# Performance work log

Hardware: AMD Instinct MI355X
Metric: run time of the kernel (lower is better)

The kernel has to match this reference:

```python
import jax, jax.numpy as jnp
import numpy as np
import math

D_MODEL = 1024
NUM_HEADS = 16
D_K = D_MODEL // NUM_HEADS
SEQ = 4096
THETA = 10000.0


def _rope_tables(d_k, max_seq_len, theta):
    freqs = 1.0 / theta ** (jnp.arange(0, d_k, 2, dtype=jnp.float32) / d_k)  # (d_k/2,)
    pos = jnp.arange(max_seq_len, dtype=jnp.float32)
    ang = pos[:, None] * freqs[None, :]  # (S, d_k/2)
    return jnp.cos(ang), jnp.sin(ang)


def setup_inputs() -> dict:
    key = jax.random.key(0)
    ks = jax.random.split(key, 5)
    std = math.sqrt(2.0 / (D_MODEL + D_MODEL))
    def trunc_w(k):
        return jax.random.truncated_normal(k, -3.0, 3.0, (D_MODEL, D_MODEL), jnp.float32) * std
    x = jax.random.normal(ks[0], (1, SEQ, D_MODEL), jnp.float32)
    Wq, Wk, Wv, Wo = trunc_w(ks[1]), trunc_w(ks[2]), trunc_w(ks[3]), trunc_w(ks[4])
    cos, sin = _rope_tables(D_K, SEQ, THETA)
    positions = jnp.arange(SEQ, dtype=jnp.int32)
    return {"x": x, "Wq": Wq, "Wk": Wk, "Wv": Wv, "Wo": Wo,
            "cos": cos, "sin": sin, "positions": positions}


def _apply_rope(t, cos, sin, positions):
    # t: (b, h, s, d_k); cos/sin: (max_s, d_k/2)
    c = cos[positions][None, None]  # (1,1,s,d_k/2)
    s = sin[positions][None, None]
    x1, x2 = t[..., ::2], t[..., 1::2]
    rotated = jnp.stack([x1 * c - x2 * s, x1 * s + x2 * c], axis=-1)  # (b,h,s,d_k/2,2)
    return rotated.reshape(t.shape)


def reference(x, Wq, Wk, Wv, Wo, cos, sin, positions):
    b, s, d = x.shape
    h, dk = NUM_HEADS, D_K
    def proj(W):
        y = jnp.einsum('bsi,oi->bso', x, W)
        return y.reshape(b, s, h, dk).transpose(0, 2, 1, 3)  # (b,h,s,dk)
    Q, K, V = proj(Wq), proj(Wk), proj(Wv)
    Q = _apply_rope(Q, cos, sin, positions)
    K = _apply_rope(K, cos, sin, positions)
    scores = jnp.einsum('bhqd,bhkd->bhqk', Q, K) / math.sqrt(dk)
    causal = jnp.tril(jnp.ones((s, s), dtype=bool))
    scores = jnp.where(causal[None, None], scores, -jnp.inf)
    weights = jax.nn.softmax(scores, axis=-1)
    y = jnp.einsum('bhqk,bhkd->bhqd', weights, V)
    y = y.transpose(0, 2, 1, 3).reshape(b, s, d)
    return jnp.einsum('bsi,oi->bso', y, Wo)
```

## Files before the change

kernel.cpp:

```cpp
#include <hip/hip_runtime.h>
#include <math.h>

#define SEQ 4096
#define DM  1024
#define NH  16
#define DK  64

typedef __attribute__((ext_vector_type(4))) float f32x4;
typedef __attribute__((ext_vector_type(8))) short bf16x8;
typedef __attribute__((ext_vector_type(8))) unsigned short u16x8;

union FragU { u16x8 u; bf16x8 b; ushort4 q[2]; unsigned w[4]; };

__device__ __forceinline__ unsigned cvtpk(float a, float b) {
    unsigned r; asm("v_cvt_pk_bf16_f32 %0, %1, %2" : "=v"(r) : "v"(a), "v"(b)); return r;
}
__device__ __forceinline__ float fexp2(float x) {
    float r; asm("v_exp_f32 %0, %1" : "=v"(r) : "v"(x)); return r;
}
__device__ __forceinline__ float bf_f(unsigned short s) {
    return __uint_as_float(((unsigned)s) << 16);
}
__device__ __forceinline__ void split4(float4 v, ushort4& hv, ushort4& lv) {
    union { ushort4 q; unsigned w[2]; } H, L;
    H.w[0] = cvtpk(v.x, v.y); H.w[1] = cvtpk(v.z, v.w);
    const float rx = v.x - __uint_as_float(H.w[0] << 16);
    const float ry = v.y - __uint_as_float(H.w[0] & 0xffff0000u);
    const float rz = v.z - __uint_as_float(H.w[1] << 16);
    const float rw = v.w - __uint_as_float(H.w[1] & 0xffff0000u);
    L.w[0] = cvtpk(rx, ry); L.w[1] = cvtpk(rz, rw);
    hv = H.q; lv = L.q;
}
__device__ __forceinline__ void split1(float f, unsigned short& h, unsigned short& l) {
    const unsigned hw = cvtpk(f, f) & 0xffffu;
    h = (unsigned short)hw;
    const float r = f - __uint_as_float(hw << 16);
    l = (unsigned short)(__float_as_uint(r) >> 16);
}

__global__ __launch_bounds__(256)
void split_f32(const float* __restrict__ src, unsigned short* __restrict__ hi,
               unsigned short* __restrict__ lo, int n4)
{
    const int stride = gridDim.x * 256;
    for (int i = blockIdx.x * 256 + threadIdx.x; i < n4; i += stride) {
        const float4 v = reinterpret_cast<const float4*>(src)[i];
        ushort4 hv, lv;
        split4(v, hv, lv);
        reinterpret_cast<ushort4*>(hi)[i] = hv;
        reinterpret_cast<ushort4*>(lo)[i] = lv;
    }
}

template<int MODE>
__global__ __launch_bounds__(256, 2)
void gemm_mfma(const unsigned short* __restrict__ Ahi, const unsigned short* __restrict__ Alo,
               const float* __restrict__ W0, const float* __restrict__ W1,
               const float* __restrict__ W2,
               unsigned short* __restrict__ OQh, unsigned short* __restrict__ OQl,
               unsigned short* __restrict__ OKh, unsigned short* __restrict__ OKl,
               unsigned short* __restrict__ OVh,
               float* __restrict__ Ofp,
               const float* __restrict__ cosT, const float* __restrict__ sinT,
               const int* __restrict__ positions)
{
    constexpr int NT = (MODE == 4) ? 24 : 8;
    __shared__ unsigned short As[128][76];
    __shared__ unsigned short Bs[128][76];

    const int t   = threadIdx.x;
    const int bid = blockIdx.x;
    const int qpx = (32 * NT) >> 3;
    const int swz = (bid & 7) * qpx + (bid >> 3);
    const int by  = swz / NT;
    const int bxf = swz % NT;
    const int wt  = (MODE == 4) ? (bxf >> 3) : 0;
    const int bx  = (MODE == 4) ? (bxf & 7) : bxf;
    const int m0  = by * 128;
    const float* W = (MODE == 4) ? (wt == 0 ? W0 : (wt == 1 ? W1 : W2)) : W0;

    const int lane = t & 63, w = t >> 6;
    const int wr = w >> 1, wc = w & 1;
    const int l15 = lane & 15, lg = lane >> 4;

    const int ar = t >> 1, ah = t & 1;
    const unsigned short* Aph = &Ahi[(size_t)(m0 + ar) * DM + ah * 16];
    const unsigned short* Apl = &Alo[(size_t)(m0 + ar) * DM + ah * 16];
    const float* Wp = &W[(size_t)(bx * 128 + ar) * DM + ah * 16];

    f32x4 acc[4][4];
#pragma unroll
    for (int mi = 0; mi < 4; ++mi)
#pragma unroll
        for (int ni = 0; ni < 4; ++ni) acc[mi][ni] = (f32x4){0.f, 0.f, 0.f, 0.f};

    float4 pb[4];
    u16x8 pah[2], pal[2];
    pah[0] = *reinterpret_cast<const u16x8*>(Aph);
    pah[1] = *reinterpret_cast<const u16x8*>(Aph + 8);
    pal[0] = *reinterpret_cast<const u16x8*>(Apl);
    pal[1] = *reinterpret_cast<const u16x8*>(Apl + 8);
#pragma unroll
    for (int g = 0; g < 4; ++g) pb[g] = *reinterpret_cast<const float4*>(Wp + g * 4);

    for (int kt = 0; kt < 32; ++kt) {
        {
            FragU h0, h1, l0, l1;
            h0.u = pah[0]; h1.u = pah[1]; l0.u = pal[0]; l1.u = pal[1];
            *reinterpret_cast<ushort4*>(&As[ar][0  + 4 * ah]) = h0.q[0];
            *reinterpret_cast<ushort4*>(&As[ar][8  + 4 * ah]) = h0.q[1];
            *reinterpret_cast<ushort4*>(&As[ar][16 + 4 * ah]) = h1.q[0];
            *reinterpret_cast<ushort4*>(&As[ar][24 + 4 * ah]) = h1.q[1];
            *reinterpret_cast<ushort4*>(&As[ar][32 + 4 * ah]) = l0.q[0];
            *reinterpret_cast<ushort4*>(&As[ar][40 + 4 * ah]) = l0.q[1];
            *reinterpret_cast<ushort4*>(&As[ar][48 + 4 * ah]) = l1.q[0];
            *reinterpret_cast<ushort4*>(&As[ar][56 + 4 * ah]) = l1.q[1];
        }
#pragma unroll
        for (int g = 0; g < 4; ++g) {
            ushort4 hv, lv;
            split4(pb[g], hv, lv);
            *reinterpret_cast<ushort4*>(&Bs[ar][8 * g + 4 * ah])      = hv;
            *reinterpret_cast<ushort4*>(&Bs[ar][32 + 8 * g + 4 * ah]) = lv;
        }
        __syncthreads();

        if (kt < 31) {
            const int ko = (kt + 1) * 32;
            pah[0] = *reinterpret_cast<const u16x8*>(Aph + ko);
            pah[1] = *reinterpret_cast<const u16x8*>(Aph + ko + 8);
            pal[0] = *reinterpret_cast<const u16x8*>(Apl + ko);
            pal[1] = *reinterpret_cast<const u16x8*>(Apl + ko + 8);
#pragma unroll
            for (int g = 0; g < 4; ++g)
                pb[g] = *reinterpret_cast<const float4*>(Wp + ko + g * 4);
        }

        FragU b_h[4], b_l[4];
#pragma unroll
        for (int ni = 0; ni < 4; ++ni) {
            const int row = wc * 64 + ni * 16 + l15;
            b_h[ni].u = *reinterpret_cast<const u16x8*>(&Bs[row][8 * lg]);
            b_l[ni].u = *reinterpret_cast<const u16x8*>(&Bs[row][32 + 8 * lg]);
        }
#pragma unroll
        for (int mi = 0; mi < 4; ++mi) {
            FragU a_h, a_l;
            const int row = wr * 64 + mi * 16 + l15;
            a_h.u = *reinterpret_cast<const u16x8*>(&As[row][8 * lg]);
            a_l.u = *reinterpret_cast<const u16x8*>(&As[row][32 + 8 * lg]);
#pragma unroll
            for (int ni = 0; ni < 4; ++ni) {
                f32x4 c = acc[mi][ni];
                c = __builtin_amdgcn_mfma_f32_16x16x32_bf16(a_h.b, b_h[ni].b, c, 0, 0, 0);
                c = __builtin_amdgcn_mfma_f32_16x16x32_bf16(a_h.b, b_l[ni].b, c, 0, 0, 0);
                c = __builtin_amdgcn_mfma_f32_16x16x32_bf16(a_l.b, b_h[ni].b, c, 0, 0, 0);
                acc[mi][ni] = c;
            }
        }
        __syncthreads();
    }

    if constexpr (MODE == 0) {
#pragma unroll
        for (int mi = 0; mi < 4; ++mi)
#pragma unroll
            for (int ni = 0; ni < 4; ++ni)
#pragma unroll
                for (int r = 0; r < 4; ++r) {
                    const int m = m0 + wr * 64 + mi * 16 + lg * 4 + r;
                    const int n = bx * 128 + wc * 64 + ni * 16 + l15;
                    Ofp[(size_t)m * DM + n] = acc[mi][ni][r];
                }
    } else if (wt == 2) {
#pragma unroll
        for (int mi = 0; mi < 4; ++mi)
#pragma unroll
            for (int ni = 0; ni < 4; ++ni) {
                ushort4 hv;
                unsigned short* hp_ = (unsigned short*)&hv;
#pragma unroll
                for (int r = 0; r < 4; ++r)
                    hp_[r] = (unsigned short)(cvtpk(acc[mi][ni][r], acc[mi][ni][r]) & 0xffffu);
                const int vrow = bx * 128 + wc * 64 + ni * 16 + l15;
                const size_t off = (size_t)vrow * SEQ + m0 + wr * 64 + mi * 16 + lg * 4;
                *reinterpret_cast<ushort4*>(&OVh[off]) = hv;
            }
    } else {
        unsigned short* Oh = (wt == 0) ? OQh : OKh;
        unsigned short* Ol = (wt == 0) ? OQl : OKl;
        const int head = bx * 2 + wc;
        const float qsc = 0.1803368801f;
#pragma unroll
        for (int mi = 0; mi < 4; ++mi)
#pragma unroll
            for (int r = 0; r < 4; ++r) {
                const int m   = m0 + wr * 64 + mi * 16 + lg * 4 + r;
                const int pos = positions[m];
#pragma unroll
                for (int ni = 0; ni < 4; ++ni) {
                    float val = acc[mi][ni][r];
                    const int d = ni * 16 + l15;
                    const float other = __shfl_xor(val, 1);
                    const float cc = cosT[pos * 32 + ni * 8 + (l15 >> 1)];
                    const float ss = sinT[pos * 32 + ni * 8 + (l15 >> 1)];
                    val = (d & 1) ? fmaf(other, ss, val * cc)
                                  : fmaf(other, -ss, val * cc);
                    if (wt == 0) val *= qsc;
                    unsigned short hh, ll;
                    split1(val, hh, ll);
                    const size_t off = ((size_t)head * SEQ + m) * DK + d;
                    Oh[off] = hh; Ol[off] = ll;
                }
            }
    }
}

__global__ __launch_bounds__(256, 2)
void attn_mfma(const unsigned short* __restrict__ Qhi, const unsigned short* __restrict__ Qlo,
               const unsigned short* __restrict__ Khi, const unsigned short* __restrict__ Klo,
               const unsigned short* __restrict__ Vhi,
               unsigned short* __restrict__ Yh, unsigned short* __restrict__ Yl,
               unsigned short* __restrict__ Pb,
               float2* __restrict__ mlA, float2* __restrict__ mlB)
{
    __shared__ unsigned short KsH[2][64][64], KsL[2][64][64], Vs[2][64][64];

    const int t = threadIdx.x, lane = t & 63, w = t >> 6;
    const int bid  = blockIdx.x;
    const int xcd  = bid & 7;
    const int s    = bid >> 3;
    const int hl   = s & 1;
    const int slot = s >> 1;
    const int p    = slot & 15;
    const int half = slot >> 4;
    const int h    = 2 * xcd + hl;

    const int l15 = lane & 15, lg = lane >> 4, dg = lg * 4;
    const int srow = t >> 2, q16 = t & 3;
    const int wh = w & 1;

    int wcol[4];
#pragma unroll
    for (int m = 0; m < 4; ++m) {
        const int g = (q16 >> 1) * 4 + m;
        wcol[m] = (((g ^ (srow & 7)) << 3) + ((q16 & 1) << 2));
    }

    u16x8 pf[6];
    auto PREFETCH = [&](int ktn) {
        const size_t gK = ((size_t)h * SEQ + (size_t)ktn * 64 + srow) * DK + q16 * 16;
        const size_t gV = ((size_t)h * DK + srow) * SEQ + (size_t)ktn * 64 + q16 * 16;
        pf[0] = *reinterpret_cast<const u16x8*>(&Khi[gK]);
        pf[1] = *reinterpret_cast<const u16x8*>(&Khi[gK + 8]);
        pf[2] = *reinterpret_cast<const u16x8*>(&Klo[gK]);
        pf[3] = *reinterpret_cast<const u16x8*>(&Klo[gK + 8]);
        pf[4] = *reinterpret_cast<const u16x8*>(&Vhi[gV]);
        pf[5] = *reinterpret_cast<const u16x8*>(&Vhi[gV + 8]);
    };
    auto STAGE = [&](int b) {
        FragU f;
        f.u = pf[0];
        *reinterpret_cast<ushort4*>(&KsH[b][srow][wcol[0]]) = f.q[0];
        *reinterpret_cast<ushort4*>(&KsH[b][srow][wcol[1]]) = f.q[1];
        f.u = pf[1];
        *reinterpret_cast<ushort4*>(&KsH[b][srow][wcol[2]]) = f.q[0];
        *reinterpret_cast<ushort4*>(&KsH[b][srow][wcol[3]]) = f.q[1];
        f.u = pf[2];
        *reinterpret_cast<ushort4*>(&KsL[b][srow][wcol[0]]) = f.q[0];
        *reinterpret_cast<ushort4*>(&KsL[b][srow][wcol[1]]) = f.q[1];
        f.u = pf[3];
        *reinterpret_cast<ushort4*>(&KsL[b][srow][wcol[2]]) = f.q[0];
        *reinterpret_cast<ushort4*>(&KsL[b][srow][wcol[3]]) = f.q[1];
        f.u = pf[4];
        *reinterpret_cast<ushort4*>(&Vs[b][srow][wcol[0]]) = f.q[0];
        *reinterpret_cast<ushort4*>(&Vs[b][srow][wcol[1]]) = f.q[1];
        f.u = pf[5];
        *reinterpret_cast<ushort4*>(&Vs[b][srow][wcol[2]]) = f.q[0];
        *reinterpret_cast<ushort4*>(&Vs[b][srow][wcol[3]]) = f.q[1];
    };

    const int nph = (half == 0) ? 2 : 1;
#pragma unroll 1
    for (int ph = 0; ph < nph; ++ph) {
        const int qt    = (half == 0 && ph == 0) ? p : (31 - p);
        const int kt0   = (half == 1) ? (31 - 2 * p) : 0;
        const int kt1   = (half == 0) ? ((ph == 0) ? (2 * p + 2) : (31 - 2 * p))
                                      : (64 - 2 * p);
        const int emode = (half == 0) ? ph : 2;
        const int diagkt = 2 * qt + (w >> 1);

        bf16x8 qh[2][2], ql[2][2];
#pragma unroll
        for (int u = 0; u < 2; ++u) {
            const size_t qrow = ((size_t)h * SEQ + (size_t)qt * 128 + w * 32 + u * 16 + l15) * DK;
#pragma unroll
            for (int c = 0; c < 2; ++c) {
                FragU uh, ul;
                uh.q[0] = *reinterpret_cast<const ushort4*>(&Qhi[qrow + c * 32 + dg]);
                uh.q[1] = *reinterpret_cast<const ushort4*>(&Qhi[qrow + c * 32 + 16 + dg]);
                ul.q[0] = *reinterpret_cast<const ushort4*>(&Qlo[qrow + c * 32 + dg]);
                ul.q[1] = *reinterpret_cast<const ushort4*>(&Qlo[qrow + c * 32 + 16 + dg]);
                qh[u][c] = uh.b; ql[u][c] = ul.b;
            }
        }

        f32x4 yacc[2][4];
#pragma unroll
        for (int u = 0; u < 2; ++u)
#pragma unroll
            for (int dt = 0; dt < 4; ++dt) yacc[u][dt] = (f32x4){0.f, 0.f, 0.f, 0.f};
        float m_run[2] = {-1e30f, -1e30f}, l_run[2] = {0.f, 0.f};

        PREFETCH(kt0);
        __syncthreads();
        STAGE(0);
        if (kt0 + 1 < kt1) PREFETCH(kt0 + 1);

        for (int kt = kt0; kt < kt1; ++kt) {
            const int b = (kt - kt0) & 1;
            __syncthreads();
            if (kt + 1 < kt1) {
                STAGE(b ^ 1);
                if (kt + 2 < kt1) PREFETCH(kt + 2);
            }

            if (kt <= diagkt) {
                const bool diag = (kt == diagkt);

                f32x4 st[2][4];
#pragma unroll
                for (int ktile = 0; ktile < 4; ++ktile) {
                    const int rowK = ktile * 16 + l15;
                    const int swk  = rowK & 7;
                    FragU kh0, kl0, kh1, kl1;
                    {
                        const int p0 = ((0 + lg) ^ swk) << 3;
                        const int p1 = ((4 + lg) ^ swk) << 3;
                        kh0.u = *reinterpret_cast<const u16x8*>(&KsH[b][rowK][p0]);
                        kl0.u = *reinterpret_cast<const u16x8*>(&KsL[b][rowK][p0]);
                        kh1.u = *reinterpret_cast<const u16x8*>(&KsH[b][rowK][p1]);
                        kl1.u = *reinterpret_cast<const u16x8*>(&KsL[b][rowK][p1]);
                    }
#pragma unroll
                    for (int u = 0; u < 2; ++u) {
                        if (diag && ktile > wh * 2 + u) {
                            st[u][ktile] = (f32x4){-1e30f, -1e30f, -1e30f, -1e30f};
                            continue;
                        }
                        f32x4 s0 = (f32x4){0.f, 0.f, 0.f, 0.f};
                        s0 = __builtin_amdgcn_mfma_f32_16x16x32_bf16(kh0.b, qh[u][0], s0, 0, 0, 0);
                        s0 = __builtin_amdgcn_mfma_f32_16x16x32_bf16(kh0.b, ql[u][0], s0, 0, 0, 0);
                        s0 = __builtin_amdgcn_mfma_f32_16x16x32_bf16(kl0.b, qh[u][0], s0, 0, 0, 0);
                        s0 = __builtin_amdgcn_mfma_f32_16x16x32_bf16(kh1.b, qh[u][1], s0, 0, 0, 0);
                        s0 = __builtin_amdgcn_mfma_f32_16x16x32_bf16(kh1.b, ql[u][1], s0, 0, 0, 0);
                        s0 = __builtin_amdgcn_mfma_f32_16x16x32_bf16(kl1.b, qh[u][1], s0, 0, 0, 0);
                        st[u][ktile] = s0;
                    }
                }

                if (diag) {
#pragma unroll
                    for (int u = 0; u < 2; ++u) {
                        const int ub = wh * 2 + u;
#pragma unroll
                        for (int r = 0; r < 4; ++r)
                            if (dg + r > l15) st[u][ub][r] = -1e30f;
                    }
                }

                bf16x8 pa[2][2];
#pragma unroll
                for (int u = 0; u < 2; ++u) {
                    float rowmax = st[u][0][0];
#pragma unroll
                    for (int ktile = 0; ktile < 4; ++ktile)
#pragma unroll
                        for (int r = 0; r < 4; ++r) rowmax = fmaxf(rowmax, st[u][ktile][r]);
                    rowmax = fmaxf(rowmax, __shfl_xor(rowmax, 16));
                    rowmax = fmaxf(rowmax, __shfl_xor(rowmax, 32));
                    if (!__all(rowmax <= m_run[u] + 11.5f)) {
                        const float mnew = fmaxf(m_run[u], rowmax);
                        const float factor = fexp2(m_run[u] - mnew);
                        l_run[u] *= factor;
#pragma unroll
                        for (int r = 0; r < 4; ++r) {
                            const float fr = __shfl(factor, (lg << 2) | r);
#pragma unroll
                            for (int dt = 0; dt < 4; ++dt) yacc[u][dt][r] *= fr;
                        }
                        m_run[u] = mnew;
                    }
                    float pp[4][4]; float psum = 0.f;
#pragma unroll
                    for (int ktile = 0; ktile < 4; ++ktile)
#pragma unroll
                        for (int r = 0; r < 4; ++r) {
                            pp[ktile][r] = fexp2(st[u][ktile][r] - m_run[u]);
                            psum += pp[ktile][r];
                        }
                    psum += __shfl_xor(psum, 16);
                    psum += __shfl_xor(psum, 32);
                    l_run[u] += psum;
#pragma unroll
                    for (int c = 0; c < 2; ++c) {
                        FragU P;
                        P.w[0] = cvtpk(pp[2 * c][0],     pp[2 * c][1]);
                        P.w[1] = cvtpk(pp[2 * c][2],     pp[2 * c][3]);
                        P.w[2] = cvtpk(pp[2 * c + 1][0], pp[2 * c + 1][1]);
                        P.w[3] = cvtpk(pp[2 * c + 1][2], pp[2 * c + 1][3]);
                        pa[u][c] = P.b;
                    }
                }

#pragma unroll
                for (int dt = 0; dt < 4; ++dt) {
                    const int rowV = dt * 16 + l15;
                    const int swv  = rowV & 7;
#pragma unroll
                    for (int c = 0; c < 2; ++c) {
                        FragU vh;
                        vh.u = *reinterpret_cast<const u16x8*>(&Vs[b][rowV][((c * 4 + lg) ^ swv) << 3]);
#pragma unroll
                        for (int u = 0; u < 2; ++u) {
                            if (diag && c == 1 && (wh * 2 + u) < 2) continue;
                            yacc[u][dt] = __builtin_amdgcn_mfma_f32_16x16x32_bf16(pa[u][c], vh.b, yacc[u][dt], 0, 0, 0);
                        }
                    }
                }
            }
        }

        if (emode == 0) {
#pragma unroll
            for (int u = 0; u < 2; ++u) {
                const float inv = 1.0f / l_run[u];
#pragma unroll
                for (int r = 0; r < 4; ++r) {
                    const float ir = __shfl(inv, (lg << 2) | r);
                    const size_t row = (size_t)qt * 128 + w * 32 + u * 16 + lg * 4 + r;
#pragma unroll
                    for (int dt = 0; dt < 4; ++dt) {
                        unsigned short hh, ll;
                        split1(yacc[u][dt][r] * ir, hh, ll);
                        const size_t off = row * DM + h * DK + dt * 16 + l15;
                        Yh[off] = hh; Yl[off] = ll;
                    }
                }
            }
        } else if (emode == 1) {
#pragma unroll
            for (int u = 0; u < 2; ++u) {
#pragma unroll
                for (int r = 0; r < 4; ++r) {
                    const size_t row = (size_t)qt * 128 + w * 32 + u * 16 + lg * 4 + r;
#pragma unroll
                    for (int dt = 0; dt < 4; ++dt) {
                        unsigned short hh, ll;
                        split1(yacc[u][dt][r], hh, ll);
                        const size_t off = row * DM + h * DK + dt * 16 + l15;
                        Yh[off] = hh; Yl[off] = ll;
                    }
                }
                if (lane < 16)
                    mlA[(h * 16 + p) * 128 + w * 32 + u * 16 + lane] =
                        make_float2(m_run[u], l_run[u]);
            }
        } else {
#pragma unroll
            for (int u = 0; u < 2; ++u) {
#pragma unroll
                for (int r = 0; r < 4; ++r) {
                    const int rloc = w * 32 + u * 16 + lg * 4 + r;
#pragma unroll
                    for (int dt = 0; dt < 4; ++dt) {
                        Pb[((size_t)(h * 16 + p) * 128 + rloc) * 64 + dt * 16 + l15] =
                            (unsigned short)(cvtpk(yacc[u][dt][r], yacc[u][dt][r]) & 0xffffu);
                    }
                }
                if (lane < 16)
                    mlB[(h * 16 + p) * 128 + w * 32 + u * 16 + lane] =
                        make_float2(m_run[u], l_run[u]);
            }
        }
    }
}

__global__ __launch_bounds__(256)
void merge_heavy(unsigned short* __restrict__ Yh, unsigned short* __restrict__ Yl,
                 const unsigned short* __restrict__ Pb,
                 const float2* __restrict__ mlA, const float2* __restrict__ mlB)
{
    const int hp = blockIdx.x;
    const int h = hp >> 4, p = hp & 15;
    const int t = threadIdx.x;
    const int row = t >> 1;
    const int d0 = (t & 1) * 32;
    const float2 a = mlA[hp * 128 + row];
    const float2 b = mlB[hp * 128 + row];
    const float m  = fmaxf(a.x, b.x);
    const float fA = fexp2(a.x - m), fB = fexp2(b.x - m);
    const float inv = 1.0f / (fA * a.y + fB * b.y);
    const size_t rg = ((size_t)(31 - p) * 128 + row) * DM + h * DK + d0;
    const size_t pg = ((size_t)hp * 128 + row) * 64 + d0;
#pragma unroll
    for (int dd = 0; dd < 32; dd += 8) {
        u16x8 vh = *reinterpret_cast<const u16x8*>(&Yh[rg + dd]);
        u16x8 vl = *reinterpret_cast<const u16x8*>(&Yl[rg + dd]);
        u16x8 vb = *reinterpret_cast<const u16x8*>(&Pb[pg + dd]);
        u16x8 oh, ol;
#pragma unroll
        for (int j = 0; j < 8; ++j) {
            const float ya = bf_f(vh[j]) + bf_f(vl[j]);
            const float yb = bf_f(vb[j]);
            const float o  = (fA * ya + fB * yb) * inv;
            unsigned short hh, ll;
            split1(o, hh, ll);
            oh[j] = hh; ol[j] = ll;
        }
        *reinterpret_cast<u16x8*>(&Yh[rg + dd]) = oh;
        *reinterpret_cast<u16x8*>(&Yl[rg + dd]) = ol;
    }
}

extern "C" void kernel_launch(void* const* d_in, const int* in_sizes, int n_in,
                              void* d_out, int out_size, void* d_ws, size_t ws_size,
                              hipStream_t stream)
{
    const float* x    = (const float*)d_in[0];
    const float* Wq   = (const float*)d_in[1];
    const float* Wk   = (const float*)d_in[2];
    const float* Wv   = (const float*)d_in[3];
    const float* Wo   = (const float*)d_in[4];
    const float* cosT = (const float*)d_in[5];
    const float* sinT = (const float*)d_in[6];
    const int*   pos  = (const int*)d_in[7];
    float* out = (float*)d_out;

    const size_t E = (size_t)SEQ * DM;
    unsigned short* xh = (unsigned short*)d_ws;
    unsigned short* xl = xh + E;
    unsigned short* qh = xl + E;
    unsigned short* ql = qh + E;
    unsigned short* kh = ql + E;
    unsigned short* kl = kh + E;
    unsigned short* vh = kl + E;
    unsigned short* Pb = vh + E;
    float2* mlA = (float2*)(Pb + (size_t)256 * 128 * 64);
    float2* mlB = mlA + (size_t)256 * 128;
    unsigned short* yh = xh;
    unsigned short* yl = xl;

    split_f32<<<dim3(1024), dim3(256), 0, stream>>>(x, xh, xl, (int)(E / 4));
    gemm_mfma<4><<<dim3(768), dim3(256), 0, stream>>>(
        xh, xl, Wq, Wk, Wv, qh, ql, kh, kl, vh, nullptr, cosT, sinT, pos);
    attn_mfma<<<dim3(512), dim3(256), 0, stream>>>(
        qh, ql, kh, kl, vh, yh, yl, Pb, mlA, mlB);
    merge_heavy<<<dim3(256), dim3(256), 0, stream>>>(yh, yl, Pb, mlA, mlB);
    gemm_mfma<0><<<dim3(256), dim3(256), 0, stream>>>(
        yh, yl, Wo, nullptr, nullptr,
        nullptr, nullptr, nullptr, nullptr, nullptr, out, cosT, sinT, pos);
}
```

Before: 275.9 us.

## Split attention KV range across three wave groups with in-block merge, drop merge kernel

The attention kernel now uses 384-thread blocks that each own a 64-row query tile in two balanced phases (p and 63-p). The KV tiles are split across three wave-pair groups, each with its own LDS slab. Partial softmax states are combined inside the block through LDS, which removes the separate merge kernel and the global round-trip of partial outputs and m/l statistics. In exchange there are extra barriers, serialized accumulation into a shared fp32 buffer, and single-buffered per-group staging without the previous double-buffer overlap.

New measurement: 584.3 us. 2.12x slower.

```diff
diff --git a/kernel.cpp b/kernel.cpp
--- a/kernel.cpp
+++ b/kernel.cpp
@@ -216,84 +216,80 @@
     }
 }
 
-__global__ __launch_bounds__(256, 2)
+__global__ __launch_bounds__(384, 3)
 void attn_mfma(const unsigned short* __restrict__ Qhi, const unsigned short* __restrict__ Qlo,
                const unsigned short* __restrict__ Khi, const unsigned short* __restrict__ Klo,
                const unsigned short* __restrict__ Vhi,
-               unsigned short* __restrict__ Yh, unsigned short* __restrict__ Yl,
-               unsigned short* __restrict__ Pb,
-               float2* __restrict__ mlA, float2* __restrict__ mlB)
+               unsigned short* __restrict__ Yh, unsigned short* __restrict__ Yl)
 {
-    __shared__ unsigned short KsH[2][64][64], KsL[2][64][64], Vs[2][64][64];
-
-    const int t = threadIdx.x, lane = t & 63, w = t >> 6;
+    __shared__ unsigned short KsH[3][64][64], KsL[3][64][64], Vs[3][64][64];
+    __shared__ float2 mlLds[3][64];
+
+    const int t    = threadIdx.x;
+    const int lane = t & 63;
+    const int wave = t >> 6;
+    const int g    = wave >> 1;
+    const int w_in = wave & 1;
     const int bid  = blockIdx.x;
-    const int xcd  = bid & 7;
-    const int s    = bid >> 3;
-    const int hl   = s & 1;
-    const int slot = s >> 1;
-    const int p    = slot & 15;
-    const int half = slot >> 4;
-    const int h    = 2 * xcd + hl;
+    const int h    = 2 * (bid & 7) + ((bid >> 3) & 1);
+    const int p    = bid >> 4;
 
     const int l15 = lane & 15, lg = lane >> 4, dg = lg * 4;
-    const int srow = t >> 2, q16 = t & 3;
-    const int wh = w & 1;
-
-    int wcol[4];
-#pragma unroll
-    for (int m = 0; m < 4; ++m) {
-        const int g = (q16 >> 1) * 4 + m;
-        wcol[m] = (((g ^ (srow & 7)) << 3) + ((q16 & 1) << 2));
-    }
-
-    u16x8 pf[6];
-    auto PREFETCH = [&](int ktn) {
-        const size_t gK = ((size_t)h * SEQ + (size_t)ktn * 64 + srow) * DK + q16 * 16;
-        const size_t gV = ((size_t)h * DK + srow) * SEQ + (size_t)ktn * 64 + q16 * 16;
-        pf[0] = *reinterpret_cast<const u16x8*>(&Khi[gK]);
-        pf[1] = *reinterpret_cast<const u16x8*>(&Khi[gK + 8]);
-        pf[2] = *reinterpret_cast<const u16x8*>(&Klo[gK]);
-        pf[3] = *reinterpret_cast<const u16x8*>(&Klo[gK + 8]);
-        pf[4] = *reinterpret_cast<const u16x8*>(&Vhi[gV]);
-        pf[5] = *reinterpret_cast<const u16x8*>(&Vhi[gV + 8]);
+    const int gt   = t & 127;
+    const int srow = gt >> 1;
+    const int ch   = gt & 1;
+
+    int woff[4];
+#pragma unroll
+    for (int m = 0; m < 4; ++m)
+        woff[m] = srow * 64 + (((ch * 4 + m) ^ (srow & 7)) << 3);
+
+    unsigned short* ksh = &KsH[g][0][0];
+    unsigned short* ksl = &KsL[g][0][0];
+    unsigned short* vs  = &Vs[g][0][0];
+
+    u16x8 pf[12];
+    auto PREFETCH = [&](int kt) {
+        const size_t gK = ((size_t)h * SEQ + (size_t)kt * 64 + srow) * DK + ch * 32;
+        const size_t gV = ((size_t)h * DK + srow) * SEQ + (size_t)kt * 64 + ch * 32;
+#pragma unroll
+        for (int m = 0; m < 4; ++m) {
+            pf[m]     = *reinterpret_cast<const u16x8*>(&Khi[gK + m * 8]);
+            pf[4 + m] = *reinterpret_cast<const u16x8*>(&Klo[gK + m * 8]);
+            pf[8 + m] = *reinterpret_cast<const u16x8*>(&Vhi[gV + m * 8]);
+        }
     };
-    auto STAGE = [&](int b) {
-        FragU f;
-        f.u = pf[0];
-        *reinterpret_cast<ushort4*>(&KsH[b][srow][wcol[0]]) = f.q[0];
-        *reinterpret_cast<ushort4*>(&KsH[b][srow][wcol[1]]) = f.q[1];
-        f.u = pf[1];
-        *reinterpret_cast<ushort4*>(&KsH[b][srow][wcol[2]]) = f.q[0];
-        *reinterpret_cast<ushort4*>(&KsH[b][srow][wcol[3]]) = f.q[1];
-        f.u = pf[2];
-        *reinterpret_cast<ushort4*>(&KsL[b][srow][wcol[0]]) = f.q[0];
-        *reinterpret_cast<ushort4*>(&KsL[b][srow][wcol[1]]) = f.q[1];
-        f.u = pf[3];
-        *reinterpret_cast<ushort4*>(&KsL[b][srow][wcol[2]]) = f.q[0];
-        *reinterpret_cast<ushort4*>(&KsL[b][srow][wcol[3]]) = f.q[1];
-        f.u = pf[4];
-        *reinterpret_cast<ushort4*>(&Vs[b][srow][wcol[0]]) = f.q[0];
-        *reinterpret_cast<ushort4*>(&Vs[b][srow][wcol[1]]) = f.q[1];
-        f.u = pf[5];
-        *reinterpret_cast<ushort4*>(&Vs[b][srow][wcol[2]]) = f.q[0];
-        *reinterpret_cast<ushort4*>(&Vs[b][srow][wcol[3]]) = f.q[1];
+    auto STAGE = [&]() {
+#pragma unroll
+        for (int arr = 0; arr < 3; ++arr) {
+            unsigned short* dst = (arr == 0) ? ksh : ((arr == 1) ? ksl : vs);
+#pragma unroll
+            for (int m = 0; m < 4; ++m) {
+                FragU lo, hi, gr;
+                lo.u = pf[arr * 4 + (m >> 1)];
+                hi.u = pf[arr * 4 + 2 + (m >> 1)];
+                gr.q[0] = lo.q[m & 1];
+                gr.q[1] = hi.q[m & 1];
+                *reinterpret_cast<u16x8*>(&dst[woff[m]]) = gr.u;
+            }
+        }
     };
 
-    const int nph = (half == 0) ? 2 : 1;
+    const int rb0 = w_in * 2;
+
 #pragma unroll 1
-    for (int ph = 0; ph < nph; ++ph) {
-        const int qt    = (half == 0 && ph == 0) ? p : (31 - p);
-        const int kt0   = (half == 1) ? (31 - 2 * p) : 0;
-        const int kt1   = (half == 0) ? ((ph == 0) ? (2 * p + 2) : (31 - 2 * p))
-                                      : (64 - 2 * p);
-        const int emode = (half == 0) ? ph : 2;
-        const int diagkt = 2 * qt + (w >> 1);
+    for (int phase = 0; phase < 2; ++phase) {
+        const int qt     = phase ? (63 - p) : p;
+        const int ntiles = qt + 1;
+        const int nq     = ntiles / 3, rq = ntiles % 3;
+        const int n_g    = nq + (g < rq ? 1 : 0);
+        const int base   = g * nq + (g < rq ? g : rq);
+        const int iters  = nq + (rq ? 1 : 0);
 
         bf16x8 qh[2][2], ql[2][2];
 #pragma unroll
         for (int u = 0; u < 2; ++u) {
-            const size_t qrow = ((size_t)h * SEQ + (size_t)qt * 128 + w * 32 + u * 16 + l15) * DK;
+            const size_t qrow = ((size_t)h * SEQ + (size_t)qt * 64 + w_in * 32 + u * 16 + l15) * DK;
 #pragma unroll
             for (int c = 0; c < 2; ++c) {
                 FragU uh, ul;
@@ -312,21 +308,17 @@
             for (int dt = 0; dt < 4; ++dt) yacc[u][dt] = (f32x4){0.f, 0.f, 0.f, 0.f};
         float m_run[2] = {-1e30f, -1e30f}, l_run[2] = {0.f, 0.f};
 
-        PREFETCH(kt0);
-        __syncthreads();
-        STAGE(0);
-        if (kt0 + 1 < kt1) PREFETCH(kt0 + 1);
-
-        for (int kt = kt0; kt < kt1; ++kt) {
-            const int b = (kt - kt0) & 1;
+        if (n_g > 0) PREFETCH(base);
+
+        for (int it = 0; it < iters; ++it) {
             __syncthreads();
-            if (kt + 1 < kt1) {
-                STAGE(b ^ 1);
-                if (kt + 2 < kt1) PREFETCH(kt + 2);
-            }
-
-            if (kt <= diagkt) {
-                const bool diag = (kt == diagkt);
+            if (it < n_g) STAGE();
+            __syncthreads();
+            if (it + 1 < n_g) PREFETCH(base + it + 1);
+
+            if (it < n_g) {
+                const int kt   = base + it;
+                const bool diag = (kt == qt);
 
                 f32x4 st[2][4];
 #pragma unroll
@@ -337,14 +329,14 @@
                     {
                         const int p0 = ((0 + lg) ^ swk) << 3;
                         const int p1 = ((4 + lg) ^ swk) << 3;
-                        kh0.u = *reinterpret_cast<const u16x8*>(&KsH[b][rowK][p0]);
-                        kl0.u = *reinterpret_cast<const u16x8*>(&KsL[b][rowK][p0]);
-                        kh1.u = *reinterpret_cast<const u16x8*>(&KsH[b][rowK][p1]);
-                        kl1.u = *reinterpret_cast<const u16x8*>(&KsL[b][rowK][p1]);
+                        kh0.u = *reinterpret_cast<const u16x8*>(&ksh[rowK * 64 + p0]);
+                        kl0.u = *reinterpret_cast<const u16x8*>(&ksl[rowK * 64 + p0]);
+                        kh1.u = *reinterpret_cast<const u16x8*>(&ksh[rowK * 64 + p1]);
+                        kl1.u = *reinterpret_cast<const u16x8*>(&ksl[rowK * 64 + p1]);
                     }
 #pragma unroll
                     for (int u = 0; u < 2; ++u) {
-                        if (diag && ktile > wh * 2 + u) {
+                        if (diag && ktile > rb0 + u) {
                             st[u][ktile] = (f32x4){-1e30f, -1e30f, -1e30f, -1e30f};
                             continue;
                         }
@@ -362,7 +354,7 @@
                 if (diag) {
 #pragma unroll
                     for (int u = 0; u < 2; ++u) {
-                        const int ub = wh * 2 + u;
+                        const int ub = rb0 + u;
 #pragma unroll
                         for (int r = 0; r < 4; ++r)
                             if (dg + r > l15) st[u][ub][r] = -1e30f;
@@ -420,10 +412,10 @@
 #pragma unroll
                     for (int c = 0; c < 2; ++c) {
                         FragU vh;
-                        vh.u = *reinterpret_cast<const u16x8*>(&Vs[b][rowV][((c * 4 + lg) ^ swv) << 3]);
+                        vh.u = *reinterpret_cast<const u16x8*>(&vs[rowV * 64 + (((c * 4 + lg) ^ swv) << 3)]);
 #pragma unroll
                         for (int u = 0; u < 2; ++u) {
-                            if (diag && c == 1 && (wh * 2 + u) < 2) continue;
+                            if (diag && c == 1 && (rb0 + u) < 2) continue;
                             yacc[u][dt] = __builtin_amdgcn_mfma_f32_16x16x32_bf16(pa[u][c], vh.b, yacc[u][dt], 0, 0, 0);
                         }
                     }
@@ -431,95 +423,72 @@
             }
         }
 
-        if (emode == 0) {
-#pragma unroll
-            for (int u = 0; u < 2; ++u) {
-                const float inv = 1.0f / l_run[u];
-#pragma unroll
-                for (int r = 0; r < 4; ++r) {
-                    const float ir = __shfl(inv, (lg << 2) | r);
-                    const size_t row = (size_t)qt * 128 + w * 32 + u * 16 + lg * 4 + r;
-#pragma unroll
-                    for (int dt = 0; dt < 4; ++dt) {
-                        unsigned short hh, ll;
-                        split1(yacc[u][dt][r] * ir, hh, ll);
-                        const size_t off = row * DM + h * DK + dt * 16 + l15;
-                        Yh[off] = hh; Yl[off] = ll;
-                    }
-                }
-            }
-        } else if (emode == 1) {
-#pragma unroll
-            for (int u = 0; u < 2; ++u) {
-#pragma unroll
-                for (int r = 0; r < 4; ++r) {
-                    const size_t row = (size_t)qt * 128 + w * 32 + u * 16 + lg * 4 + r;
-#pragma unroll
-                    for (int dt = 0; dt < 4; ++dt) {
-                        unsigned short hh, ll;
-                        split1(yacc[u][dt][r], hh, ll);
-                        const size_t off = row * DM + h * DK + dt * 16 + l15;
-                        Yh[off] = hh; Yl[off] = ll;
-                    }
-                }
-                if (lane < 16)
-                    mlA[(h * 16 + p) * 128 + w * 32 + u * 16 + lane] =
-                        make_float2(m_run[u], l_run[u]);
-            }
-        } else {
-#pragma unroll
-            for (int u = 0; u < 2; ++u) {
-#pragma unroll
-                for (int r = 0; r < 4; ++r) {
-                    const int rloc = w * 32 + u * 16 + lg * 4 + r;
-#pragma unroll
-                    for (int dt = 0; dt < 4; ++dt) {
-                        Pb[((size_t)(h * 16 + p) * 128 + rloc) * 64 + dt * 16 + l15] =
-                            (unsigned short)(cvtpk(yacc[u][dt][r], yacc[u][dt][r]) & 0xffffu);
-                    }
-                }
-                if (lane < 16)
-                    mlB[(h * 16 + p) * 128 + w * 32 + u * 16 + lane] =
-                        make_float2(m_run[u], l_run[u]);
-            }
-        }
-    }
-}
-
-__global__ __launch_bounds__(256)
-void merge_heavy(unsigned short* __restrict__ Yh, unsigned short* __restrict__ Yl,
-                 const unsigned short* __restrict__ Pb,
-                 const float2* __restrict__ mlA, const float2* __restrict__ mlB)
-{
-    const int hp = blockIdx.x;
-    const int h = hp >> 4, p = hp & 15;
-    const int t = threadIdx.x;
-    const int row = t >> 1;
-    const int d0 = (t & 1) * 32;
-    const float2 a = mlA[hp * 128 + row];
-    const float2 b = mlB[hp * 128 + row];
-    const float m  = fmaxf(a.x, b.x);
-    const float fA = fexp2(a.x - m), fB = fexp2(b.x - m);
-    const float inv = 1.0f / (fA * a.y + fB * b.y);
-    const size_t rg = ((size_t)(31 - p) * 128 + row) * DM + h * DK + d0;
-    const size_t pg = ((size_t)hp * 128 + row) * 64 + d0;
-#pragma unroll
-    for (int dd = 0; dd < 32; dd += 8) {
-        u16x8 vh = *reinterpret_cast<const u16x8*>(&Yh[rg + dd]);
-        u16x8 vl = *reinterpret_cast<const u16x8*>(&Yl[rg + dd]);
-        u16x8 vb = *reinterpret_cast<const u16x8*>(&Pb[pg + dd]);
-        u16x8 oh, ol;
-#pragma unroll
-        for (int j = 0; j < 8; ++j) {
-            const float ya = bf_f(vh[j]) + bf_f(vl[j]);
-            const float yb = bf_f(vb[j]);
-            const float o  = (fA * ya + fB * yb) * inv;
-            unsigned short hh, ll;
-            split1(o, hh, ll);
-            oh[j] = hh; ol[j] = ll;
-        }
-        *reinterpret_cast<u16x8*>(&Yh[rg + dd]) = oh;
-        *reinterpret_cast<u16x8*>(&Yl[rg + dd]) = ol;
+        __syncthreads();
+        if (lane < 16) {
+            mlLds[g][w_in * 32 + lane]      = make_float2(m_run[0], l_run[0]);
+            mlLds[g][w_in * 32 + 16 + lane] = make_float2(m_run[1], l_run[1]);
+        }
+        __syncthreads();
+
+        float fg[2];
+#pragma unroll
+        for (int u = 0; u < 2; ++u) {
+            const int row = w_in * 32 + u * 16 + l15;
+            const float m0 = mlLds[0][row].x;
+            const float m1 = mlLds[1][row].x;
+            const float m2 = mlLds[2][row].x;
+            const float mstar = fmaxf(fmaxf(m0, m1), m2);
+            fg[u] = fexp2(m_run[u] - mstar);
+        }
+
+        float* fbuf = (float*)&KsH[0][0][0];
+#pragma unroll 1
+        for (int gg = 0; gg < 3; ++gg) {
+            if (g == gg) {
+#pragma unroll
+                for (int u = 0; u < 2; ++u)
+#pragma unroll
+                    for (int r = 0; r < 4; ++r) {
+                        const float fr = __shfl(fg[u], (lg << 2) | r);
+                        const int row = w_in * 32 + u * 16 + lg * 4 + r;
+#pragma unroll
+                        for (int dt = 0; dt < 4; ++dt) {
+                            const int col = dt * 16 + l15;
+                            if (gg == 0) fbuf[row * 68 + col]  = yacc[u][dt][r] * fr;
+                            else         fbuf[row * 68 + col] += yacc[u][dt][r] * fr;
+                        }
+                    }
+            }
+            __syncthreads();
+        }
+
+        for (int idx = t; idx < 512; idx += 384) {
+            const int row = idx >> 3, cg = idx & 7;
+            const float2 a0 = mlLds[0][row];
+            const float2 a1 = mlLds[1][row];
+            const float2 a2 = mlLds[2][row];
+            const float mstar = fmaxf(fmaxf(a0.x, a1.x), a2.x);
+            const float denom = fexp2(a0.x - mstar) * a0.y
+                              + fexp2(a1.x - mstar) * a1.y
+                              + fexp2(a2.x - mstar) * a2.y;
+            const float inv = 1.0f / denom;
+            ushort4 oh[2], ol[2];
+#pragma unroll
+            for (int half = 0; half < 2; ++half) {
+                unsigned short* hp_ = (unsigned short*)&oh[half];
+                unsigned short* lp_ = (unsigned short*)&ol[half];
+#pragma unroll
+                for (int j = 0; j < 4; ++j) {
+                    const float o = fbuf[row * 68 + cg * 8 + half * 4 + j] * inv;
+                    split1(o, hp_[j], lp_[j]);
+                }
+            }
+            const size_t off = ((size_t)qt * 64 + row) * DM + h * DK + cg * 8;
+            *reinterpret_cast<ushort4*>(&Yh[off])     = oh[0];
+            *reinterpret_cast<ushort4*>(&Yh[off + 4]) = oh[1];
+            *reinterpret_cast<ushort4*>(&Yl[off])     = ol[0];
+            *reinterpret_cast<ushort4*>(&Yl[off + 4]) = ol[1];
+        }
     }
 }
 
@@ -545,18 +514,14 @@
     unsigned short* kh = ql + E;
     unsigned short* kl = kh + E;
     unsigned short* vh = kl + E;
-    unsigned short* Pb = vh + E;
-    float2* mlA = (float2*)(Pb + (size_t)256 * 128 * 64);
-    float2* mlB = mlA + (size_t)256 * 128;
     unsigned short* yh = xh;
     unsigned short* yl = xl;
 
     split_f32<<<dim3(1024), dim3(256), 0, stream>>>(x, xh, xl, (int)(E / 4));
     gemm_mfma<4><<<dim3(768), dim3(256), 0, stream>>>(
         xh, xl, Wq, Wk, Wv, qh, ql, kh, kl, vh, nullptr, cosT, sinT, pos);
-    attn_mfma<<<dim3(512), dim3(256), 0, stream>>>(
-        qh, ql, kh, kl, vh, yh, yl, Pb, mlA, mlB);
-    merge_heavy<<<dim3(256), dim3(256), 0, stream>>>(yh, yl, Pb, mlA, mlB);
+    attn_mfma<<<dim3(512), dim3(384), 0, stream>>>(
+        qh, ql, kh, kl, vh, yh, yl);
     gemm_mfma<0><<<dim3(256), dim3(256), 0, stream>>>(
         yh, yl, Wo, nullptr, nullptr,
         nullptr, nullptr, nullptr, nullptr, nullptr, out, cosT, sinT, pos);
```
